# Performance work log

Hardware: AMD Instinct MI355X
Metric: run time of the kernel (lower is better)

Reference implementation:

```python
import jax, jax.numpy as jnp
import numpy as np

N, E, G = 100000, 1600000, 100
NEG_SLOPE = 0.2
EPS = 1e-5


def gatv2_conv(x, src, dst, Wl, Wr, att, bias, concat):
    # PyG GATv2Conv (eval mode, add_self_loops already applied to src/dst).
    # x: [N, F_in]; Wl/Wr: [F_in, H*C]; att: [H, C]; bias: [H*C] or [C].
    H, C = att.shape
    n = x.shape[0]
    xl = (x @ Wl).reshape(n, H, C)  # source-side transform (messages)
    xr = (x @ Wr).reshape(n, H, C)  # target-side transform
    m = jax.nn.leaky_relu(xl[src] + xr[dst], NEG_SLOPE)      # [Etot, H, C]
    e = jnp.einsum('ehc,hc->eh', m, att)                      # [Etot, H]
    # softmax over incoming edges of each destination node (per head)
    emax = jax.ops.segment_max(e, dst, num_segments=n)        # [n, H]
    ex = jnp.exp(e - emax[dst])
    denom = jax.ops.segment_sum(ex, dst, num_segments=n)
    alpha = ex / denom[dst]                                   # [Etot, H]
    out = jax.ops.segment_sum(xl[src] * alpha[..., None], dst, num_segments=n)  # [n, H, C]
    out = out.reshape(n, H * C) if concat else out.mean(axis=1)
    return out + bias


def graph_norm(x, batch, w, b, mean_scale):
    # PyG GraphNorm: per-graph mean/var with learnable mean_scale.
    cnt = jnp.maximum(jax.ops.segment_sum(jnp.ones((x.shape[0], 1), x.dtype), batch, num_segments=G), 1.0)
    mean = jax.ops.segment_sum(x, batch, num_segments=G) / cnt
    xc = x - mean_scale * mean[batch]
    var = jax.ops.segment_sum(xc * xc, batch, num_segments=G) / cnt
    return w * xc / jnp.sqrt(var[batch] + EPS) + b


def global_mean_pool(x, batch):
    cnt = jnp.maximum(jax.ops.segment_sum(jnp.ones((x.shape[0], 1), x.dtype), batch, num_segments=G), 1.0)
    return jax.ops.segment_sum(x, batch, num_segments=G) / cnt


def setup_inputs() -> dict:
    key = jax.random.key(0)
    ks = jax.random.split(key, 16)
    F_in, H, C12, C3 = 64, 4, 16, 32
    s_in = 1.0 / np.sqrt(F_in)
    s_h = 1.0 / np.sqrt(H * C12)
    inp = {
        'x': jax.random.normal(ks[0], (N, F_in), jnp.float32),
        'edge_index': jax.random.randint(ks[1], (2, E), 0, N, jnp.int64),
        'batch': jnp.sort(jax.random.randint(ks[2], (N,), 0, G, jnp.int64)),
        'Wl1': jax.random.normal(ks[3], (F_in, H * C12), jnp.float32) * s_in,
        'Wr1': jax.random.normal(ks[4], (F_in, H * C12), jnp.float32) * s_in,
        'att1': jax.random.normal(ks[5], (H, C12), jnp.float32) * s_in,
        'b1': jnp.zeros((H * C12,), jnp.float32),
        'g1w': jnp.ones((H * C12,), jnp.float32),
        'g1b': jnp.zeros((H * C12,), jnp.float32),
        'g1a': jnp.ones((H * C12,), jnp.float32),
        'Wl2': jax.random.normal(ks[6], (H * C12, H * C12), jnp.float32) * s_h,
        'Wr2': jax.random.normal(ks[7], (H * C12, H * C12), jnp.float32) * s_h,
        'att2': jax.random.normal(ks[8], (H, C12), jnp.float32) * s_h,
        'b2': jnp.zeros((H * C12,), jnp.float32),
        'g2w': jnp.ones((H * C12,), jnp.float32),
        'g2b': jnp.zeros((H * C12,), jnp.float32),
        'g2a': jnp.ones((H * C12,), jnp.float32),
        'Wl3': jax.random.normal(ks[9], (H * C12, H * C3), jnp.float32) * s_h,
        'Wr3': jax.random.normal(ks[10], (H * C12, H * C3), jnp.float32) * s_h,
        'att3': jax.random.normal(ks[11], (H, C3), jnp.float32) * s_h,
        'b3': jnp.zeros((C3,), jnp.float32),
        'g3w': jnp.ones((C3,), jnp.float32),
        'g3b': jnp.zeros((C3,), jnp.float32),
        'g3a': jnp.ones((C3,), jnp.float32),
        'Wlin': jax.random.normal(ks[12], (C3, 2), jnp.float32) * (1.0 / np.sqrt(C3)),
        'blin': jnp.zeros((2,), jnp.float32),
    }
    return inp


def reference(x, edge_index, batch, Wl1, Wr1, att1, b1, g1w, g1b, g1a,
              Wl2, Wr2, att2, b2, g2w, g2b, g2a,
              Wl3, Wr3, att3, b3, g3w, g3b, g3a, Wlin, blin):
    # add self-loops (GATv2Conv default)
    loops = jnp.arange(N, dtype=edge_index.dtype)
    src = jnp.concatenate([edge_index[0], loops])
    dst = jnp.concatenate([edge_index[1], loops])
    h = jax.nn.relu(graph_norm(gatv2_conv(x, src, dst, Wl1, Wr1, att1, b1, True), batch, g1w, g1b, g1a))
    h = jax.nn.relu(graph_norm(gatv2_conv(h, src, dst, Wl2, Wr2, att2, b2, True), batch, g2w, g2b, g2a))
    h = jax.nn.relu(graph_norm(gatv2_conv(h, src, dst, Wl3, Wr3, att3, b3, False), batch, g3w, g3b, g3a))
    pooled = global_mean_pool(h, batch)  # [G, h3]
    return pooled @ Wlin + blin          # [G, 2]
```

## Files before the change

### kernel.cpp

```cpp
#include <hip/hip_runtime.h>
#include <hip/hip_bf16.h>

#define LEAKY 0.2f
#define EPS_GN 1e-5f
#define PSH 9

typedef unsigned int uint;
typedef __attribute__((ext_vector_type(8))) short bf16x8;
typedef __attribute__((ext_vector_type(4))) float f32x4;


__device__ inline float4 bf4(uint lo, uint hi) {
    union { uint u; float f; } a, b, c, d;
    a.u = lo << 16; b.u = lo & 0xFFFF0000u;
    c.u = hi << 16; d.u = hi & 0xFFFF0000u;
    return make_float4(a.f, b.f, c.f, d.f);
}

__device__ inline uint pack_bf2(float lo, float hi) {
    union { float f; uint u; } x, y; x.f = lo; y.f = hi;
    uint ra = x.u + 0x7FFFu + ((x.u >> 16) & 1u);
    uint rb = y.u + 0x7FFFu + ((y.u >> 16) & 1u);
    return (ra >> 16) | (rb & 0xFFFF0000u);
}

__device__ inline unsigned short pack_bf1(float v) {
    union { float f; uint u; } q; q.f = v;
    return (unsigned short)((q.u + 0x7FFFu + ((q.u >> 16) & 1u)) >> 16);
}


__global__ void zero_int_kernel(int* __restrict__ p, int n) {
    int i = blockIdx.x * blockDim.x + threadIdx.x;
    if (i < n) p[i] = 0;
}

__global__ void hist_kernel(const int* __restrict__ dst, int* __restrict__ deg, int E_, int Etot_) {
    int i = blockIdx.x * blockDim.x + threadIdx.x;
    if (i >= Etot_) return;
    int d = (i < E_) ? dst[i] : (i - E_);
    atomicAdd(&deg[d], 1);
}

__global__ void scan1_kernel(const int* __restrict__ deg, int* __restrict__ bsum, int nN) {
    __shared__ int sd[256];
    int i = blockIdx.x * 256 + threadIdx.x;
    sd[threadIdx.x] = (i < nN) ? deg[i] : 0;
    __syncthreads();
    for (int off = 128; off > 0; off >>= 1) {
        if (threadIdx.x < off) sd[threadIdx.x] += sd[threadIdx.x + off];
        __syncthreads();
    }
    if (threadIdx.x == 0) bsum[blockIdx.x] = sd[0];
}

__global__ void scan2_kernel(const int* __restrict__ bsum, int* __restrict__ bofs, int nb,
                             int* __restrict__ rowstart, int nN, int* __restrict__ csr_pad) {
    __shared__ int sd[512];
    int tid = threadIdx.x;
    int v = (tid < nb) ? bsum[tid] : 0;
    sd[tid] = v;
    __syncthreads();
    for (int off = 1; off < 512; off <<= 1) {
        int t = (tid >= off) ? sd[tid - off] : 0;
        __syncthreads();
        sd[tid] += t;
        __syncthreads();
    }
    if (tid < nb) bofs[tid] = sd[tid] - v;
    if (tid == 511) rowstart[nN] = sd[511];
    if (tid < 16) csr_pad[tid] = 0;
}

__global__ void scan3_kernel(const int* __restrict__ deg, const int* __restrict__ bofs,
                             int* __restrict__ rowstart, int nN) {
    __shared__ int sd[256];
    int i = blockIdx.x * 256 + threadIdx.x;
    int v = (i < nN) ? deg[i] : 0;
    sd[threadIdx.x] = v;
    __syncthreads();
    for (int off = 1; off < 256; off <<= 1) {
        int t = (threadIdx.x >= off) ? sd[threadIdx.x - off] : 0;
        __syncthreads();
        sd[threadIdx.x] += t;
        __syncthreads();
    }
    if (i < nN) rowstart[i] = bofs[blockIdx.x] + sd[threadIdx.x] - v;
}

__global__ void init_gcur_kernel(const int* __restrict__ rowstart, int* __restrict__ gcur,
                                 int P, int nN) {
    int p = blockIdx.x * blockDim.x + threadIdx.x;
    if (p > P) return;
    int node = p << PSH;
    if (node > nN) node = nN;
    gcur[p] = rowstart[node];
}

__global__ void partA_kernel(const int* __restrict__ srcs, const int* __restrict__ dsts,
                             int* __restrict__ gcur, uint* __restrict__ ebuf,
                             int E_, int Etot_) {
    __shared__ int hist[256], base_s[256], lcur[256];
    int tid = threadIdx.x;
    hist[tid] = 0; lcur[tid] = 0;
    __syncthreads();
    int i0 = blockIdx.x * 2048 + tid;
    uint rec[8]; int pp[8];
#pragma unroll
    for (int k = 0; k < 8; ++k) {
        int i = i0 + k * 256;
        pp[k] = -1;
        if (i < Etot_) {
            int s, d;
            if (i < E_) { s = srcs[i]; d = dsts[i]; } else { s = i - E_; d = s; }
            int p = d >> PSH;
            pp[k] = p;
            rec[k] = (uint)s | ((uint)(d & ((1 << PSH) - 1)) << 17);
            atomicAdd(&hist[p], 1);
        }
    }
    __syncthreads();
    int h = hist[tid];
    if (h > 0) base_s[tid] = atomicAdd(&gcur[tid], h);
    __syncthreads();
#pragma unroll
    for (int k = 0; k < 8; ++k) {
        if (pp[k] >= 0) {
            int pos = base_s[pp[k]] + atomicAdd(&lcur[pp[k]], 1);
            ebuf[pos] = rec[k];
        }
    }
}

__global__ void partB_kernel(const uint* __restrict__ ebuf, const int* __restrict__ rowstart,
                             int* __restrict__ csr, int nN) {
    __shared__ int lcur[512];
    int tid = threadIdx.x;
    lcur[tid] = 0; lcur[tid + 256] = 0;
    __syncthreads();
    int n0 = blockIdx.x << PSH;
    int n1 = n0 + (1 << PSH);
    if (n1 > nN) n1 = nN;
    int lo = rowstart[n0], hi = rowstart[n1];
    const int* rs = rowstart + n0;
    for (int i = lo + tid; i < hi; i += 256) {
        uint v = ebuf[i];
        int dl = (int)(v >> 17);
        int pos = rs[dl] + atomicAdd(&lcur[dl], 1);
        csr[pos] = (int)(v & 0x1FFFFu);
    }
}

__global__ void goff_kernel(const int* __restrict__ batch, int* __restrict__ goff, int nN, int nG) {
    int g = blockIdx.x * blockDim.x + threadIdx.x;
    if (g > nG) return;
    if (g == nG) { goff[g] = nN; return; }
    int lo = 0, hi = nN;
    while (lo < hi) { int mid = (lo + hi) >> 1; if (batch[mid] < g) lo = mid + 1; else hi = mid; }
    goff[g] = lo;
}


__global__ void wtprep_kernel(const float* __restrict__ Wl1, const float* __restrict__ Wr1,
                              const float* __restrict__ Wl2, const float* __restrict__ Wr2,
                              const float* __restrict__ Wl3, const float* __restrict__ Wr3,
                              unsigned short* __restrict__ wt1, unsigned short* __restrict__ wt2,
                              unsigned short* __restrict__ wt3) {
    int idx = blockIdx.x * 256 + threadIdx.x;
    if (idx < 8192) {
        int col = idx >> 6, k = idx & 63;
        float v = (col < 64) ? Wl1[k * 64 + col] : Wr1[k * 64 + (col - 64)];
        wt1[col * 64 + k] = pack_bf1(v);
    } else if (idx < 16384) {
        int i = idx - 8192; int col = i >> 6, k = i & 63;
        float v = (col < 64) ? Wl2[k * 64 + col] : Wr2[k * 64 + (col - 64)];
        wt2[col * 64 + k] = pack_bf1(v);
    } else if (idx < 32768) {
        int i = idx - 16384; int col = i >> 6, k = i & 63;
        float v = (col < 128) ? Wl3[k * 128 + col] : Wr3[k * 128 + (col - 128)];
        wt3[col * 64 + k] = pack_bf1(v);
    }
}


template <int NCOLS, bool NORM>
__global__ __launch_bounds__(256, 4)
void gemm_mfma_kernel(const float* __restrict__ x, const unsigned short* __restrict__ Wt,
                      unsigned short* __restrict__ xl, unsigned short* __restrict__ xr,
                      int nN, const float* __restrict__ param, const int* __restrict__ batch) {
    constexpr int NT = NCOLS / 16;
    constexpr int OD = NCOLS / 2;
    __shared__ unsigned short Xs[64 * 64];
    __shared__ unsigned short Ws[NCOLS * 64];
    int tid = threadIdx.x;
    int node0 = blockIdx.x * 64;

    {
        int nl = tid >> 2, k0 = (tid & 3) * 16;
        int n = node0 + nl;
        bool v = n < nN;
        int nc = v ? n : 0;
        const float* xrow = x + (size_t)nc * 64 + k0;
        const float* scp = nullptr; const float* shp = nullptr;
        if constexpr (NORM) {
            int g = batch[nc];
            scp = param + (size_t)g * 128 + k0;
            shp = param + (size_t)g * 128 + 64 + k0;
        }
        uint q[8];
#pragma unroll
        for (int j = 0; j < 8; ++j) {
            float a = v ? xrow[j * 2] : 0.f;
            float b = v ? xrow[j * 2 + 1] : 0.f;
            if constexpr (NORM) {
                a = fmaxf(fmaf(scp[j * 2], a, shp[j * 2]), 0.f);
                b = fmaxf(fmaf(scp[j * 2 + 1], b, shp[j * 2 + 1]), 0.f);
            }
            q[j] = pack_bf2(a, b);
        }
        char* base = (char*)Xs + nl * 128;
        uint sw = (uint)(nl & 7) << 4;
        *(uint4*)(base + (((uint)(k0 * 2)) ^ sw))      = make_uint4(q[0], q[1], q[2], q[3]);
        *(uint4*)(base + (((uint)(k0 * 2 + 16)) ^ sw)) = make_uint4(q[4], q[5], q[6], q[7]);
    }
    for (int ch = tid; ch < NCOLS * 8; ch += 256) {
        int col = ch >> 3, sub = ch & 7;
        uint4 q = ((const uint4*)(Wt + col * 64))[sub];
        *(uint4*)((char*)Ws + col * 128 + (((uint)(sub * 16)) ^ ((uint)(col & 7) << 4))) = q;
    }
    __syncthreads();

    int lane = tid & 63;
    int wv = tid >> 6;
    int l15 = lane & 15, quad = lane >> 4;

    bf16x8 xf[2];
    {
        int row = wv * 16 + l15;
        char* base = (char*)Xs + row * 128;
        uint sw = (uint)(row & 7) << 4;
        xf[0] = *(bf16x8*)(base + (((uint)(quad * 16)) ^ sw));
        xf[1] = *(bf16x8*)(base + (((uint)(64 + quad * 16)) ^ sw));
    }
    f32x4 acc[NT];
#pragma unroll
    for (int t = 0; t < NT; ++t) acc[t] = (f32x4){0.f, 0.f, 0.f, 0.f};
#pragma unroll
    for (int t = 0; t < NT; ++t) {
        int col = t * 16 + l15;
        char* base = (char*)Ws + col * 128;
        uint sw = (uint)(col & 7) << 4;
        bf16x8 a0 = *(bf16x8*)(base + (((uint)(quad * 16)) ^ sw));
        bf16x8 a1 = *(bf16x8*)(base + (((uint)(64 + quad * 16)) ^ sw));
        acc[t] = __builtin_amdgcn_mfma_f32_16x16x32_bf16(a0, xf[0], acc[t], 0, 0, 0);
        acc[t] = __builtin_amdgcn_mfma_f32_16x16x32_bf16(a1, xf[1], acc[t], 0, 0, 0);
    }
    int node = node0 + wv * 16 + l15;
    if (node < nN) {
#pragma unroll
        for (int t = 0; t < NT; ++t) {
            int cg = t * 16 + quad * 4;
            unsigned short* outp = (cg < OD) ? xl : xr;
            int ocol = (cg < OD) ? cg : cg - OD;
            uint2 pk;
            pk.x = pack_bf2(acc[t][0], acc[t][1]);
            pk.y = pack_bf2(acc[t][2], acc[t][3]);
            *(uint2*)(outp + (size_t)node * OD + ocol) = pk;
        }
    }
}


__global__ void agg64_kernel(const unsigned short* __restrict__ xl, const unsigned short* __restrict__ xr,
                             const int* __restrict__ rowstart, const int* __restrict__ csr,
                             const float* __restrict__ att, const float* __restrict__ bias,
                             float* __restrict__ out, int nN) {
    int wid = (blockIdx.x * blockDim.x + threadIdx.x) >> 6;
    int lane = threadIdx.x & 63;
    if (wid >= nN) return;
    int c8 = lane & 7;
    int sg = lane >> 3;
    const uint4* xl4 = (const uint4*)xl;
    const float LOG2E = 1.4426950408889634f;
    float4 attA = ((const float4*)att)[c8 * 2];
    float4 attB = ((const float4*)att)[c8 * 2 + 1];
    attA.x *= LOG2E; attA.y *= LOG2E; attA.z *= LOG2E; attA.w *= LOG2E;
    attB.x *= LOG2E; attB.y *= LOG2E; attB.z *= LOG2E; attB.w *= LOG2E;
    uint4 xru = ((const uint4*)xr)[(size_t)wid * 8 + c8];
    float4 xrA = bf4(xru.x, xru.y), xrB = bf4(xru.z, xru.w);
    int rs = rowstart[wid], re = rowstart[wid + 1];
    int nIt = (re - rs + 7) >> 3;
    float den = 0.f;
    float4 accA = make_float4(0.f, 0.f, 0.f, 0.f);
    float4 accB = make_float4(0.f, 0.f, 0.f, 0.f);
    int i = rs + sg;
    int s = csr[i];
    uint4 xv = xl4[(size_t)s * 8 + c8];
    for (int it = 0; it < nIt; ++it) {
        float4 curA = bf4(xv.x, xv.y), curB = bf4(xv.z, xv.w);
        bool vv = i < re;
        i += 8;
        s = csr[i];
        xv = xl4[(size_t)s * 8 + c8];
        float4 mA, mB;
        mA.x = curA.x + xrA.x; mA.y = curA.y + xrA.y;
        mA.z = curA.z + xrA.z; mA.w = curA.w + xrA.w;
        mB.x = curB.x + xrB.x; mB.y = curB.y + xrB.y;
        mB.z = curB.z + xrB.z; mB.w = curB.w + xrB.w;
        mA.x = fmaxf(mA.x, LEAKY * mA.x); mA.y = fmaxf(mA.y, LEAKY * mA.y);
        mA.z = fmaxf(mA.z, LEAKY * mA.z); mA.w = fmaxf(mA.w, LEAKY * mA.w);
        mB.x = fmaxf(mB.x, LEAKY * mB.x); mB.y = fmaxf(mB.y, LEAKY * mB.y);
        mB.z = fmaxf(mB.z, LEAKY * mB.z); mB.w = fmaxf(mB.w, LEAKY * mB.w);
        float p = mA.x * attA.x;
        p = fmaf(mA.y, attA.y, p); p = fmaf(mA.z, attA.z, p); p = fmaf(mA.w, attA.w, p);
        p = fmaf(mB.x, attB.x, p); p = fmaf(mB.y, attB.y, p);
        p = fmaf(mB.z, attB.z, p); p = fmaf(mB.w, attB.w, p);
        p += __shfl_xor(p, 1);
        float w = vv ? exp2f(p) : 0.f;
        den += w;
        accA.x = fmaf(w, curA.x, accA.x); accA.y = fmaf(w, curA.y, accA.y);
        accA.z = fmaf(w, curA.z, accA.z); accA.w = fmaf(w, curA.w, accA.w);
        accB.x = fmaf(w, curB.x, accB.x); accB.y = fmaf(w, curB.y, accB.y);
        accB.z = fmaf(w, curB.z, accB.z); accB.w = fmaf(w, curB.w, accB.w);
    }
#pragma unroll
    for (int off = 8; off <= 32; off <<= 1) {
        den    += __shfl_xor(den, off);
        accA.x += __shfl_xor(accA.x, off); accA.y += __shfl_xor(accA.y, off);
        accA.z += __shfl_xor(accA.z, off); accA.w += __shfl_xor(accA.w, off);
        accB.x += __shfl_xor(accB.x, off); accB.y += __shfl_xor(accB.y, off);
        accB.z += __shfl_xor(accB.z, off); accB.w += __shfl_xor(accB.w, off);
    }
    if (lane < 8) {
        float4 bvA = ((const float4*)bias)[c8 * 2];
        float4 bvB = ((const float4*)bias)[c8 * 2 + 1];
        float inv = 1.f / den;
        float4 rA, rB;
        rA.x = fmaf(accA.x, inv, bvA.x); rA.y = fmaf(accA.y, inv, bvA.y);
        rA.z = fmaf(accA.z, inv, bvA.z); rA.w = fmaf(accA.w, inv, bvA.w);
        rB.x = fmaf(accB.x, inv, bvB.x); rB.y = fmaf(accB.y, inv, bvB.y);
        rB.z = fmaf(accB.z, inv, bvB.z); rB.w = fmaf(accB.w, inv, bvB.w);
        ((float4*)out)[(size_t)wid * 16 + c8 * 2]     = rA;
        ((float4*)out)[(size_t)wid * 16 + c8 * 2 + 1] = rB;
    }
}


__global__ void agg128_mean_kernel(const unsigned short* __restrict__ xl, const unsigned short* __restrict__ xr,
                                   const int* __restrict__ rowstart, const int* __restrict__ csr,
                                   const float* __restrict__ att, const float* __restrict__ bias,
                                   float* __restrict__ out, int nN) {
    int wid = (blockIdx.x * blockDim.x + threadIdx.x) >> 6;
    int lane = threadIdx.x & 63;
    if (wid >= nN) return;
    int c8 = lane & 15;
    int sg = lane >> 4;
    const uint4* xl4 = (const uint4*)xl;
    const float LOG2E = 1.4426950408889634f;
    float4 attA = ((const float4*)att)[c8 * 2];
    float4 attB = ((const float4*)att)[c8 * 2 + 1];
    attA.x *= LOG2E; attA.y *= LOG2E; attA.z *= LOG2E; attA.w *= LOG2E;
    attB.x *= LOG2E; attB.y *= LOG2E; attB.z *= LOG2E; attB.w *= LOG2E;
    uint4 xru = ((const uint4*)xr)[(size_t)wid * 16 + c8];
    float4 xrA = bf4(xru.x, xru.y), xrB = bf4(xru.z, xru.w);
    int rs = rowstart[wid], re = rowstart[wid + 1];
    int nIt = (re - rs + 3) >> 2;
    float den = 0.f;
    float4 accA = make_float4(0.f, 0.f, 0.f, 0.f);
    float4 accB = make_float4(0.f, 0.f, 0.f, 0.f);
    int i = rs + sg;
    int s = csr[i];
    uint4 xv = xl4[(size_t)s * 16 + c8];
    for (int it = 0; it < nIt; ++it) {
        float4 curA = bf4(xv.x, xv.y), curB = bf4(xv.z, xv.w);
        bool vv = i < re;
        i += 4;
        s = csr[i];
        xv = xl4[(size_t)s * 16 + c8];
        float4 mA, mB;
        mA.x = curA.x + xrA.x; mA.y = curA.y + xrA.y;
        mA.z = curA.z + xrA.z; mA.w = curA.w + xrA.w;
        mB.x = curB.x + xrB.x; mB.y = curB.y + xrB.y;
        mB.z = curB.z + xrB.z; mB.w = curB.w + xrB.w;
        mA.x = fmaxf(mA.x, LEAKY * mA.x); mA.y = fmaxf(mA.y, LEAKY * mA.y);
        mA.z = fmaxf(mA.z, LEAKY * mA.z); mA.w = fmaxf(mA.w, LEAKY * mA.w);
        mB.x = fmaxf(mB.x, LEAKY * mB.x); mB.y = fmaxf(mB.y, LEAKY * mB.y);
        mB.z = fmaxf(mB.z, LEAKY * mB.z); mB.w = fmaxf(mB.w, LEAKY * mB.w);
        float p = mA.x * attA.x;
        p = fmaf(mA.y, attA.y, p); p = fmaf(mA.z, attA.z, p); p = fmaf(mA.w, attA.w, p);
        p = fmaf(mB.x, attB.x, p); p = fmaf(mB.y, attB.y, p);
        p = fmaf(mB.z, attB.z, p); p = fmaf(mB.w, attB.w, p);
        p += __shfl_xor(p, 1);
        p += __shfl_xor(p, 2);
        float w = vv ? exp2f(p) : 0.f;
        den += w;
        accA.x = fmaf(w, curA.x, accA.x); accA.y = fmaf(w, curA.y, accA.y);
        accA.z = fmaf(w, curA.z, accA.z); accA.w = fmaf(w, curA.w, accA.w);
        accB.x = fmaf(w, curB.x, accB.x); accB.y = fmaf(w, curB.y, accB.y);
        accB.z = fmaf(w, curB.z, accB.z); accB.w = fmaf(w, curB.w, accB.w);
    }
#pragma unroll
    for (int off = 16; off <= 32; off <<= 1) {
        den    += __shfl_xor(den, off);
        accA.x += __shfl_xor(accA.x, off); accA.y += __shfl_xor(accA.y, off);
        accA.z += __shfl_xor(accA.z, off); accA.w += __shfl_xor(accA.w, off);
        accB.x += __shfl_xor(accB.x, off); accB.y += __shfl_xor(accB.y, off);
        accB.z += __shfl_xor(accB.z, off); accB.w += __shfl_xor(accB.w, off);
    }
    float inv = 1.f / den;
    float4 rA, rB;
    rA.x = accA.x * inv; rA.y = accA.y * inv; rA.z = accA.z * inv; rA.w = accA.w * inv;
    rB.x = accB.x * inv; rB.y = accB.y * inv; rB.z = accB.z * inv; rB.w = accB.w * inv;
#pragma unroll
    for (int off = 4; off <= 8; off <<= 1) {
        rA.x += __shfl_xor(rA.x, off); rA.y += __shfl_xor(rA.y, off);
        rA.z += __shfl_xor(rA.z, off); rA.w += __shfl_xor(rA.w, off);
        rB.x += __shfl_xor(rB.x, off); rB.y += __shfl_xor(rB.y, off);
        rB.z += __shfl_xor(rB.z, off); rB.w += __shfl_xor(rB.w, off);
    }
    if (lane < 4) {
        float4 bvA = ((const float4*)bias)[lane * 2];
        float4 bvB = ((const float4*)bias)[lane * 2 + 1];
        float4 oA, oB;
        oA.x = fmaf(rA.x, 0.25f, bvA.x); oA.y = fmaf(rA.y, 0.25f, bvA.y);
        oA.z = fmaf(rA.z, 0.25f, bvA.z); oA.w = fmaf(rA.w, 0.25f, bvA.w);
        oB.x = fmaf(rB.x, 0.25f, bvB.x); oB.y = fmaf(rB.y, 0.25f, bvB.y);
        oB.z = fmaf(rB.z, 0.25f, bvB.z); oB.w = fmaf(rB.w, 0.25f, bvB.w);
        ((float4*)out)[(size_t)wid * 8 + lane * 2]     = oA;
        ((float4*)out)[(size_t)wid * 8 + lane * 2 + 1] = oB;
    }
}


template <int D>
__global__ void gnorm_stats_kernel(const float* __restrict__ in, const int* __restrict__ goff,
                                   float* __restrict__ stats, int SPLIT) {
    int g = blockIdx.x / SPLIT, part = blockIdx.x % SPLIT;
    int start = goff[g], end = goff[g + 1];
    constexpr int RPB = 256 / D;
    int tid = threadIdx.x;
    int c = tid % D, sub = tid / D;
    float s1 = 0.f, s2 = 0.f;
    for (int n = start + part * RPB + sub; n < end; n += SPLIT * RPB) {
        float v = in[(size_t)n * D + c];
        s1 += v; s2 += v * v;
    }
    __shared__ float l1[256], l2[256];
    l1[tid] = s1; l2[tid] = s2;
    __syncthreads();
    if (tid < D) {
        for (int s = 1; s < RPB; ++s) { s1 += l1[s * D + tid]; s2 += l2[s * D + tid]; }
        atomicAdd(&stats[(size_t)g * 2 * D + tid], s1);
        atomicAdd(&stats[(size_t)g * 2 * D + D + tid], s2);
    }
}

template <int D>
__global__ void gnorm_finalize_kernel(const float* __restrict__ stats, const int* __restrict__ goff,
                                      const float* __restrict__ w, const float* __restrict__ b,
                                      const float* __restrict__ a, float* __restrict__ param) {
    int g = blockIdx.x, c = threadIdx.x;
    if (c >= D) return;
    int cn = goff[g + 1] - goff[g];
    float cnt = (float)(cn > 1 ? cn : 1);
    float S1 = stats[(size_t)g * 2 * D + c], S2 = stats[(size_t)g * 2 * D + D + c];
    float mu = S1 / cnt;
    float am = a[c] * mu;
    float var = S2 / cnt - 2.f * am * mu + am * am;
    float sc = w[c] * rsqrtf(var + EPS_GN);
    param[(size_t)g * 2 * D + c] = sc;
    param[(size_t)g * 2 * D + D + c] = b[c] - sc * am;
}


__global__ void pool3_kernel(const float* __restrict__ in, const int* __restrict__ goff,
                             const float* __restrict__ param, float* __restrict__ pooled, int SPLIT) {
    int g = blockIdx.x / SPLIT, part = blockIdx.x % SPLIT;
    int start = goff[g], end = goff[g + 1];
    int tid = threadIdx.x;
    int c = tid & 31, sub = tid >> 5;
    float sc = param[(size_t)g * 64 + c], sh = param[(size_t)g * 64 + 32 + c];
    float s = 0.f;
    for (int n = start + part * 8 + sub; n < end; n += SPLIT * 8)
        s += fmaxf(fmaf(sc, in[(size_t)n * 32 + c], sh), 0.f);
    __shared__ float l[256];
    l[tid] = s;
    __syncthreads();
    if (tid < 32) {
        for (int q = 1; q < 8; ++q) s += l[q * 32 + tid];
        atomicAdd(&pooled[(size_t)g * 32 + tid], s);
    }
}

__global__ void lin_kernel(const float* __restrict__ pooled, const int* __restrict__ goff,
                           const float* __restrict__ Wlin, const float* __restrict__ blin,
                           float* __restrict__ out, int nG) {
    int idx = blockIdx.x * blockDim.x + threadIdx.x;
    if (idx >= nG * 2) return;
    int g = idx >> 1, o = idx & 1;
    int cn = goff[g + 1] - goff[g];
    float inv = 1.f / (float)(cn > 1 ? cn : 1);
    float acc = blin[o];
    for (int c = 0; c < 32; ++c) acc = fmaf(pooled[(size_t)g * 32 + c] * inv, Wlin[c * 2 + o], acc);
    out[idx] = acc;
}


extern "C" void kernel_launch(void* const* d_in, const int* in_sizes, int n_in,
                              void* d_out, int out_size, void* d_ws, size_t ws_size,
                              hipStream_t stream) {
    const float* x    = (const float*)d_in[0];
    const int*  eidx  = (const int*)d_in[1];
    const int*  batch = (const int*)d_in[2];
    const float* Wl1 = (const float*)d_in[3];
    const float* Wr1 = (const float*)d_in[4];
    const float* att1 = (const float*)d_in[5];
    const float* b1 = (const float*)d_in[6];
    const float* g1w = (const float*)d_in[7];
    const float* g1b = (const float*)d_in[8];
    const float* g1a = (const float*)d_in[9];
    const float* Wl2 = (const float*)d_in[10];
    const float* Wr2 = (const float*)d_in[11];
    const float* att2 = (const float*)d_in[12];
    const float* b2 = (const float*)d_in[13];
    const float* g2w = (const float*)d_in[14];
    const float* g2b = (const float*)d_in[15];
    const float* g2a = (const float*)d_in[16];
    const float* Wl3 = (const float*)d_in[17];
    const float* Wr3 = (const float*)d_in[18];
    const float* att3 = (const float*)d_in[19];
    const float* b3 = (const float*)d_in[20];
    const float* g3w = (const float*)d_in[21];
    const float* g3b = (const float*)d_in[22];
    const float* g3a = (const float*)d_in[23];
    const float* Wlin = (const float*)d_in[24];
    const float* blin = (const float*)d_in[25];
    float* outp = (float*)d_out;

    const int N = in_sizes[0] / 64;
    const int E = in_sizes[1] / 2;
    const int Etot = N + E;
    const int G = out_size / 2;
    const int NB = (N + 255) / 256;
    const int P = (N + (1 << PSH) - 1) >> PSH;
    const int SPLIT = 16;

    unsigned short* xlb = (unsigned short*)d_ws;
    unsigned short* xrb = xlb + (size_t)N * 128;
    float* agg   = (float*)(xrb + (size_t)N * 128);
    float* stats = agg + (size_t)N * 64;
    float* stats1 = stats;
    float* stats2 = stats1 + (size_t)G * 128;
    float* stats3 = stats2 + (size_t)G * 128;
    float* pooled = stats3 + (size_t)G * 64;
    float* param  = pooled + (size_t)G * 32;
    int* deg      = (int*)(param + (size_t)G * 128);
    int* rowstart = deg + N;
    int* csr      = rowstart + (N + 1);
    uint* ebuf    = (uint*)(csr + Etot + 16);
    int* bsum     = (int*)(ebuf + Etot);
    int* bofs     = bsum + NB;
    int* goff     = bofs + NB;
    int* gcur     = goff + (G + 1);
    unsigned short* wt1 = (unsigned short*)(gcur + P + 1);
    unsigned short* wt2 = wt1 + 8192;
    unsigned short* wt3 = wt2 + 8192;

    const int* src_idx = eidx;
    const int* dst_idx = eidx + E;

    zero_int_kernel<<<(N + 255) / 256, 256, 0, stream>>>(deg, N);
    zero_int_kernel<<<(G * 352 + 255) / 256, 256, 0, stream>>>((int*)stats, G * 352);
    wtprep_kernel<<<128, 256, 0, stream>>>(Wl1, Wr1, Wl2, Wr2, Wl3, Wr3, wt1, wt2, wt3);

    hist_kernel<<<(Etot + 255) / 256, 256, 0, stream>>>(dst_idx, deg, E, Etot);
    scan1_kernel<<<NB, 256, 0, stream>>>(deg, bsum, N);
    scan2_kernel<<<1, 512, 0, stream>>>(bsum, bofs, NB, rowstart, N, csr + Etot);
    scan3_kernel<<<NB, 256, 0, stream>>>(deg, bofs, rowstart, N);
    init_gcur_kernel<<<(P + 256) / 256, 256, 0, stream>>>(rowstart, gcur, P, N);
    partA_kernel<<<(Etot + 2047) / 2048, 256, 0, stream>>>(src_idx, dst_idx, gcur, ebuf, E, Etot);
    partB_kernel<<<P, 256, 0, stream>>>(ebuf, rowstart, csr, N);
    goff_kernel<<<1, 128, 0, stream>>>(batch, goff, N, G);

    dim3 blk(256);
    int aggGrid = (N + 3) / 4;
    int gemmGrid = (N + 63) / 64;

    gemm_mfma_kernel<128, false><<<gemmGrid, blk, 0, stream>>>(x, wt1, xlb, xrb, N, nullptr, nullptr);
    agg64_kernel<<<aggGrid, blk, 0, stream>>>(xlb, xrb, rowstart, csr, att1, b1, agg, N);
    gnorm_stats_kernel<64><<<G * SPLIT, blk, 0, stream>>>(agg, goff, stats1, SPLIT);
    gnorm_finalize_kernel<64><<<G, 64, 0, stream>>>(stats1, goff, g1w, g1b, g1a, param);

    gemm_mfma_kernel<128, true><<<gemmGrid, blk, 0, stream>>>(agg, wt2, xlb, xrb, N, param, batch);
    agg64_kernel<<<aggGrid, blk, 0, stream>>>(xlb, xrb, rowstart, csr, att2, b2, agg, N);
    gnorm_stats_kernel<64><<<G * SPLIT, blk, 0, stream>>>(agg, goff, stats2, SPLIT);
    gnorm_finalize_kernel<64><<<G, 64, 0, stream>>>(stats2, goff, g2w, g2b, g2a, param);

    gemm_mfma_kernel<256, true><<<gemmGrid, blk, 0, stream>>>(agg, wt3, xlb, xrb, N, param, batch);
    agg128_mean_kernel<<<aggGrid, blk, 0, stream>>>(xlb, xrb, rowstart, csr, att3, b3, agg, N);
    gnorm_stats_kernel<32><<<G * SPLIT, blk, 0, stream>>>(agg, goff, stats3, SPLIT);
    gnorm_finalize_kernel<32><<<G, 32, 0, stream>>>(stats3, goff, g3w, g3b, g3a, param);
    pool3_kernel<<<G * SPLIT, blk, 0, stream>>>(agg, goff, param, pooled, SPLIT);
    lin_kernel<<<(G * 2 + 63) / 64, 64, 0, stream>>>(pooled, goff, Wlin, blin, outp, G);
}
```

Before: 462.1 us.

## Build CSR via partition counts, computing rowstart in partB; merge setup kernels

Replaces the per-node degree histogram plus three-stage scan with a per-partition count (shared-memory histogram over 512-node buckets) and a single-block scan. Per-node row starts are now derived inside the second partition pass from local counts, and csr is filled in the same kernel. Zeroing, weight transposition, and graph offset search are merged into one setup kernel. This cuts the number of launches and removes the global atomic traffic on a 100k-entry degree array, at the cost of partB reading the edge buffer twice.

```diff
diff --git a/kernel.cpp b/kernel.cpp
--- a/kernel.cpp
+++ b/kernel.cpp
@@ -30,71 +30,92 @@
 }
 
 
-__global__ void zero_int_kernel(int* __restrict__ p, int n) {
-    int i = blockIdx.x * blockDim.x + threadIdx.x;
-    if (i < n) p[i] = 0;
-}
-
-__global__ void hist_kernel(const int* __restrict__ dst, int* __restrict__ deg, int E_, int Etot_) {
-    int i = blockIdx.x * blockDim.x + threadIdx.x;
-    if (i >= Etot_) return;
-    int d = (i < E_) ? dst[i] : (i - E_);
-    atomicAdd(&deg[d], 1);
-}
-
-__global__ void scan1_kernel(const int* __restrict__ deg, int* __restrict__ bsum, int nN) {
+__global__ void setup_kernel(float* __restrict__ stats, int statN,
+                             const float* __restrict__ Wl1, const float* __restrict__ Wr1,
+                             const float* __restrict__ Wl2, const float* __restrict__ Wr2,
+                             const float* __restrict__ Wl3, const float* __restrict__ Wr3,
+                             unsigned short* __restrict__ wt1, unsigned short* __restrict__ wt2,
+                             unsigned short* __restrict__ wt3,
+                             int* __restrict__ pcnt, int* __restrict__ csr_pad,
+                             const int* __restrict__ batch, int* __restrict__ goff,
+                             int nN, int nG) {
+    int idx = blockIdx.x * 256 + threadIdx.x;
+    if (idx < statN) { stats[idx] = 0.f; return; }
+    idx -= statN;
+    if (idx < 8192) {
+        int col = idx >> 6, k = idx & 63;
+        float v = (col < 64) ? Wl1[k * 64 + col] : Wr1[k * 64 + (col - 64)];
+        wt1[col * 64 + k] = pack_bf1(v);
+        return;
+    }
+    idx -= 8192;
+    if (idx < 8192) {
+        int col = idx >> 6, k = idx & 63;
+        float v = (col < 64) ? Wl2[k * 64 + col] : Wr2[k * 64 + (col - 64)];
+        wt2[col * 64 + k] = pack_bf1(v);
+        return;
+    }
+    idx -= 8192;
+    if (idx < 16384) {
+        int col = idx >> 6, k = idx & 63;
+        float v = (col < 128) ? Wl3[k * 128 + col] : Wr3[k * 128 + (col - 128)];
+        wt3[col * 64 + k] = pack_bf1(v);
+        return;
+    }
+    idx -= 16384;
+    if (idx < 256) { pcnt[idx] = 0; return; }
+    idx -= 256;
+    if (idx < 16) { csr_pad[idx] = 0; return; }
+    idx -= 16;
+    if (idx <= nG) {
+        if (idx == nG) { goff[idx] = nN; return; }
+        int lo = 0, hi = nN;
+        while (lo < hi) { int mid = (lo + hi) >> 1; if (batch[mid] < idx) lo = mid + 1; else hi = mid; }
+        goff[idx] = lo;
+    }
+}
+
+
+__global__ void pcount_kernel(const int* __restrict__ dsts, int* __restrict__ pcnt,
+                              int E_, int Etot_) {
+    __shared__ int h[256];
+    int tid = threadIdx.x;
+    h[tid] = 0;
+    __syncthreads();
+    int i0 = blockIdx.x * 2048 + tid;
+#pragma unroll
+    for (int k = 0; k < 8; ++k) {
+        int i = i0 + k * 256;
+        if (i < Etot_) {
+            int d = (i < E_) ? dsts[i] : (i - E_);
+            atomicAdd(&h[d >> PSH], 1);
+        }
+    }
+    __syncthreads();
+    if (h[tid] > 0) atomicAdd(&pcnt[tid], h[tid]);
+}
+
+__global__ void pscan_kernel(const int* __restrict__ pcnt, int* __restrict__ pstart,
+                             int* __restrict__ gcur, int* __restrict__ rowstart, int nN) {
     __shared__ int sd[256];
-    int i = blockIdx.x * 256 + threadIdx.x;
-    sd[threadIdx.x] = (i < nN) ? deg[i] : 0;
-    __syncthreads();
-    for (int off = 128; off > 0; off >>= 1) {
-        if (threadIdx.x < off) sd[threadIdx.x] += sd[threadIdx.x + off];
+    int t = threadIdx.x;
+    int v = pcnt[t];
+    sd[t] = v;
+    __syncthreads();
+    for (int off = 1; off < 256; off <<= 1) {
+        int tmp = (t >= off) ? sd[t - off] : 0;
         __syncthreads();
-    }
-    if (threadIdx.x == 0) bsum[blockIdx.x] = sd[0];
-}
-
-__global__ void scan2_kernel(const int* __restrict__ bsum, int* __restrict__ bofs, int nb,
-                             int* __restrict__ rowstart, int nN, int* __restrict__ csr_pad) {
-    __shared__ int sd[512];
-    int tid = threadIdx.x;
-    int v = (tid < nb) ? bsum[tid] : 0;
-    sd[tid] = v;
-    __syncthreads();
-    for (int off = 1; off < 512; off <<= 1) {
-        int t = (tid >= off) ? sd[tid - off] : 0;
+        sd[t] += tmp;
         __syncthreads();
-        sd[tid] += t;
-        __syncthreads();
-    }
-    if (tid < nb) bofs[tid] = sd[tid] - v;
-    if (tid == 511) rowstart[nN] = sd[511];
-    if (tid < 16) csr_pad[tid] = 0;
-}
-
-__global__ void scan3_kernel(const int* __restrict__ deg, const int* __restrict__ bofs,
-                             int* __restrict__ rowstart, int nN) {
-    __shared__ int sd[256];
-    int i = blockIdx.x * 256 + threadIdx.x;
-    int v = (i < nN) ? deg[i] : 0;
-    sd[threadIdx.x] = v;
-    __syncthreads();
-    for (int off = 1; off < 256; off <<= 1) {
-        int t = (threadIdx.x >= off) ? sd[threadIdx.x - off] : 0;
-        __syncthreads();
-        sd[threadIdx.x] += t;
-        __syncthreads();
-    }
-    if (i < nN) rowstart[i] = bofs[blockIdx.x] + sd[threadIdx.x] - v;
-}
-
-__global__ void init_gcur_kernel(const int* __restrict__ rowstart, int* __restrict__ gcur,
-                                 int P, int nN) {
-    int p = blockIdx.x * blockDim.x + threadIdx.x;
-    if (p > P) return;
-    int node = p << PSH;
-    if (node > nN) node = nN;
-    gcur[p] = rowstart[node];
+    }
+    int excl = sd[t] - v;
+    pstart[t] = excl;
+    gcur[t] = excl;
+    if (t == 255) {
+        pstart[256] = sd[255];
+        gcur[256] = sd[255];
+        rowstart[nN] = sd[255];
+    }
 }
 
 __global__ void partA_kernel(const int* __restrict__ srcs, const int* __restrict__ dsts,
@@ -132,53 +153,41 @@
     }
 }
 
-__global__ void partB_kernel(const uint* __restrict__ ebuf, const int* __restrict__ rowstart,
-                             int* __restrict__ csr, int nN) {
-    __shared__ int lcur[512];
-    int tid = threadIdx.x;
-    lcur[tid] = 0; lcur[tid + 256] = 0;
-    __syncthreads();
-    int n0 = blockIdx.x << PSH;
-    int n1 = n0 + (1 << PSH);
-    if (n1 > nN) n1 = nN;
-    int lo = rowstart[n0], hi = rowstart[n1];
-    const int* rs = rowstart + n0;
-    for (int i = lo + tid; i < hi; i += 256) {
+__global__ void partB2_kernel(const uint* __restrict__ ebuf, const int* __restrict__ pstart,
+                              int* __restrict__ rowstart, int* __restrict__ csr, int nN) {
+    __shared__ int cnt[512], ofs[512], ssum[256];
+    int t = threadIdx.x;
+    cnt[t] = 0; cnt[t + 256] = 0;
+    __syncthreads();
+    int p = blockIdx.x;
+    int lo = pstart[p], hi = pstart[p + 1];
+    for (int i = lo + t; i < hi; i += 256)
+        atomicAdd(&cnt[ebuf[i] >> 17], 1);
+    __syncthreads();
+    int a = cnt[2 * t], b = cnt[2 * t + 1];
+    ssum[t] = a + b;
+    __syncthreads();
+    for (int off = 1; off < 256; off <<= 1) {
+        int tmp = (t >= off) ? ssum[t - off] : 0;
+        __syncthreads();
+        ssum[t] += tmp;
+        __syncthreads();
+    }
+    int base = (t > 0) ? ssum[t - 1] : 0;
+    ofs[2 * t] = lo + base;
+    ofs[2 * t + 1] = lo + base + a;
+    __syncthreads();
+    int n0 = p << PSH;
+#pragma unroll
+    for (int j = t; j < 512; j += 256) {
+        int n = n0 + j;
+        if (n < nN) rowstart[n] = ofs[j];
+    }
+    __syncthreads();
+    for (int i = lo + t; i < hi; i += 256) {
         uint v = ebuf[i];
-        int dl = (int)(v >> 17);
-        int pos = rs[dl] + atomicAdd(&lcur[dl], 1);
+        int pos = atomicAdd(&ofs[v >> 17], 1);
         csr[pos] = (int)(v & 0x1FFFFu);
-    }
-}
-
-__global__ void goff_kernel(const int* __restrict__ batch, int* __restrict__ goff, int nN, int nG) {
-    int g = blockIdx.x * blockDim.x + threadIdx.x;
-    if (g > nG) return;
-    if (g == nG) { goff[g] = nN; return; }
-    int lo = 0, hi = nN;
-    while (lo < hi) { int mid = (lo + hi) >> 1; if (batch[mid] < g) lo = mid + 1; else hi = mid; }
-    goff[g] = lo;
-}
-
-
-__global__ void wtprep_kernel(const float* __restrict__ Wl1, const float* __restrict__ Wr1,
-                              const float* __restrict__ Wl2, const float* __restrict__ Wr2,
-                              const float* __restrict__ Wl3, const float* __restrict__ Wr3,
-                              unsigned short* __restrict__ wt1, unsigned short* __restrict__ wt2,
-                              unsigned short* __restrict__ wt3) {
-    int idx = blockIdx.x * 256 + threadIdx.x;
-    if (idx < 8192) {
-        int col = idx >> 6, k = idx & 63;
-        float v = (col < 64) ? Wl1[k * 64 + col] : Wr1[k * 64 + (col - 64)];
-        wt1[col * 64 + k] = pack_bf1(v);
-    } else if (idx < 16384) {
-        int i = idx - 8192; int col = i >> 6, k = i & 63;
-        float v = (col < 64) ? Wl2[k * 64 + col] : Wr2[k * 64 + (col - 64)];
-        wt2[col * 64 + k] = pack_bf1(v);
-    } else if (idx < 32768) {
-        int i = idx - 16384; int col = i >> 6, k = i & 63;
-        float v = (col < 128) ? Wl3[k * 128 + col] : Wr3[k * 128 + (col - 128)];
-        wt3[col * 64 + k] = pack_bf1(v);
     }
 }
 
@@ -541,7 +550,6 @@
     const int E = in_sizes[1] / 2;
     const int Etot = N + E;
     const int G = out_size / 2;
-    const int NB = (N + 255) / 256;
     const int P = (N + (1 << PSH) - 1) >> PSH;
     const int SPLIT = 16;
 
@@ -554,33 +562,31 @@
     float* stats3 = stats2 + (size_t)G * 128;
     float* pooled = stats3 + (size_t)G * 64;
     float* param  = pooled + (size_t)G * 32;
-    int* deg      = (int*)(param + (size_t)G * 128);
-    int* rowstart = deg + N;
+    int* rowstart = (int*)(param + (size_t)G * 128);
     int* csr      = rowstart + (N + 1);
     uint* ebuf    = (uint*)(csr + Etot + 16);
-    int* bsum     = (int*)(ebuf + Etot);
-    int* bofs     = bsum + NB;
-    int* goff     = bofs + NB;
+    int* goff     = (int*)(ebuf + Etot);
     int* gcur     = goff + (G + 1);
-    unsigned short* wt1 = (unsigned short*)(gcur + P + 1);
+    int* pstart   = gcur + 257;
+    int* pcnt     = pstart + 257;
+    unsigned short* wt1 = (unsigned short*)(pcnt + 256);
     unsigned short* wt2 = wt1 + 8192;
     unsigned short* wt3 = wt2 + 8192;
 
     const int* src_idx = eidx;
     const int* dst_idx = eidx + E;
 
-    zero_int_kernel<<<(N + 255) / 256, 256, 0, stream>>>(deg, N);
-    zero_int_kernel<<<(G * 352 + 255) / 256, 256, 0, stream>>>((int*)stats, G * 352);
-    wtprep_kernel<<<128, 256, 0, stream>>>(Wl1, Wr1, Wl2, Wr2, Wl3, Wr3, wt1, wt2, wt3);
-
-    hist_kernel<<<(Etot + 255) / 256, 256, 0, stream>>>(dst_idx, deg, E, Etot);
-    scan1_kernel<<<NB, 256, 0, stream>>>(deg, bsum, N);
-    scan2_kernel<<<1, 512, 0, stream>>>(bsum, bofs, NB, rowstart, N, csr + Etot);
-    scan3_kernel<<<NB, 256, 0, stream>>>(deg, bofs, rowstart, N);
-    init_gcur_kernel<<<(P + 256) / 256, 256, 0, stream>>>(rowstart, gcur, P, N);
-    partA_kernel<<<(Etot + 2047) / 2048, 256, 0, stream>>>(src_idx, dst_idx, gcur, ebuf, E, Etot);
-    partB_kernel<<<P, 256, 0, stream>>>(ebuf, rowstart, csr, N);
-    goff_kernel<<<1, 128, 0, stream>>>(batch, goff, N, G);
+    const int statN = G * 352;
+    int setupTotal = statN + 32768 + 256 + 16 + (G + 1);
+    setup_kernel<<<(setupTotal + 255) / 256, 256, 0, stream>>>(
+        stats, statN, Wl1, Wr1, Wl2, Wr2, Wl3, Wr3, wt1, wt2, wt3,
+        pcnt, csr + Etot, batch, goff, N, G);
+
+    int edgeBlocks = (Etot + 2047) / 2048;
+    pcount_kernel<<<edgeBlocks, 256, 0, stream>>>(dst_idx, pcnt, E, Etot);
+    pscan_kernel<<<1, 256, 0, stream>>>(pcnt, pstart, gcur, rowstart, N);
+    partA_kernel<<<edgeBlocks, 256, 0, stream>>>(src_idx, dst_idx, gcur, ebuf, E, Etot);
+    partB2_kernel<<<P, 256, 0, stream>>>(ebuf, pstart, rowstart, csr, N);
 
     dim3 blk(256);
     int aggGrid = (N + 3) / 4;
```

Result: faster. 409.5 us, median of 2 (-11.4%).
